# Kernel optimization log

Measured on AMD Instinct MI355X. Metric: run time of the kernel, lower is better.

Reference implementation:

```python
import jax, jax.numpy as jnp
import numpy as np

INV_SQRT2 = 0.7071067811865476


def _dense(x, W):
    return jax.nn.silu(x @ W)


def _residual(x, Wa, Wb):
    # GemNet ResidualLayer: two activated dense layers, skip, 1/sqrt(2) rescale
    return (x + _dense(_dense(x, Wa), Wb)) * INV_SQRT2


def setup_inputs() -> dict:
    key = jax.random.key(0)
    ks = iter(jax.random.split(key, 40))
    N, E, T = 10000, 200000, 400000
    NR, NS = 128, 7          # num_radial, num_spherical
    A, M, Ti, To, C = 128, 256, 64, 64, 16
    NB = 2                   # num_blocks

    def w(shape):
        fan_in = shape[-2]
        return jax.random.normal(next(ks), shape, jnp.float32) / float(np.sqrt(fan_in))

    inp = {}
    inp['atomic_numbers'] = jax.random.randint(next(ks), (N,), 0, 120)
    inp['idx_s'] = jax.random.randint(next(ks), (E,), 0, N)
    inp['idx_t'] = jax.random.randint(next(ks), (E,), 0, N)
    inp['id3_ba'] = jax.random.randint(next(ks), (T,), 0, E)
    inp['id3_ca'] = jax.random.randint(next(ks), (T,), 0, E)
    inp['rbf'] = jax.random.uniform(next(ks), (E, NR), jnp.float32)
    inp['cbf'] = jax.random.normal(next(ks), (T, NS), jnp.float32)
    V = jax.random.normal(next(ks), (E, 3), jnp.float32)
    inp['V_st'] = V / jnp.linalg.norm(V, axis=-1, keepdims=True)
    inp['atom_table'] = jax.random.normal(next(ks), (120, A), jnp.float32)
    inp['W_edge_in'] = w((2 * A + NR, M))
    inp['rbf_w3'] = w((NB, NR, M))
    inp['W_down'] = w((NB, M, Ti))
    inp['W_cbf'] = w((NB, NS, C))
    inp['W_bil'] = jax.random.normal(next(ks), (NB, C, Ti, To), jnp.float32) / float(np.sqrt(C * Ti))
    inp['W_up'] = w((NB, To, M))
    inp['W_res_e'] = w((NB, 4, M, M))
    inp['rbf_wh'] = w((NB, NR, M))
    inp['W_e2a'] = w((NB, M, A))
    inp['W_res_a'] = w((NB, 2, A, A))
    inp['W_outE_in'] = w((A * (NB + 1), A))
    inp['W_outE_res'] = w((2, A, A))
    inp['W_outE_fin'] = w((A, 1))
    inp['W_outF_in'] = w((M * (NB + 1), M))
    inp['W_outF_res'] = w((2, M, M))
    inp['W_outF_fin'] = w((M, 1))
    return inp


def reference(atomic_numbers, idx_s, idx_t, id3_ba, id3_ca, rbf, cbf, V_st,
              atom_table, W_edge_in, rbf_w3, W_down, W_cbf, W_bil, W_up,
              W_res_e, rbf_wh, W_e2a, W_res_a,
              W_outE_in, W_outE_res, W_outE_fin,
              W_outF_in, W_outF_res, W_outF_fin):
    N = atomic_numbers.shape[0]
    E = idx_s.shape[0]
    NB = rbf_w3.shape[0]

    # atom and edge embeddings
    h = atom_table[atomic_numbers]                                       # [N, A]
    m = _dense(jnp.concatenate([h[idx_s], h[idx_t], rbf], axis=-1), W_edge_in)  # [E, M]

    xs_E = [h]
    xs_F = [m]
    for b in range(NB):
        # --- triplet interaction: edge -> triplet gather, bilinear CBF mix, scatter back ---
        x = (m * (rbf @ rbf_w3[b])) @ W_down[b]                          # [E, Ti]
        cb = cbf @ W_cbf[b]                                              # [T, C]
        y = jnp.einsum('tc,ti,cio->to', cb, x[id3_ba], W_bil[b])         # [T, To]
        agg = jax.ops.segment_sum(y, id3_ca, num_segments=E)             # [E, To]
        x3 = _dense(agg @ W_up[b], jnp.eye(x3_dim := W_up[b].shape[1], dtype=m.dtype)) if False else jax.nn.silu(agg @ W_up[b])  # [E, M]
        # --- residual / skip structure ---
        m2 = _residual(m, W_res_e[b, 0], W_res_e[b, 1])
        m2 = (m2 + x3) * INV_SQRT2
        m = _residual(m2, W_res_e[b, 2], W_res_e[b, 3])
        # --- atom update: edge -> atom scatter ---
        xa = (m * (rbf @ rbf_wh[b])) @ W_e2a[b]                          # [E, A]
        ha = jax.ops.segment_sum(xa, idx_t, num_segments=N)              # [N, A]
        h = h + _residual(ha, W_res_a[b, 0], W_res_a[b, 1])
        xs_E.append(h)
        xs_F.append(m)

    # FinalMLP-style heads over concatenated per-block features (emb*(num_blocks+1))
    xE = _residual(_dense(jnp.concatenate(xs_E, axis=-1), W_outE_in), W_outE_res[0], W_outE_res[1])
    E_atom = xE @ W_outE_fin                                             # [N, 1]
    xF = _residual(_dense(jnp.concatenate(xs_F, axis=-1), W_outF_in), W_outF_res[0], W_outF_res[1])
    F_edge = xF @ W_outF_fin                                             # [E, 1]
    forces = jax.ops.segment_sum(F_edge * V_st, idx_t, num_segments=N)   # [N, 3]
    return jnp.concatenate([E_atom, forces], axis=-1)                    # [N, 4]
```

## Files before the change

### kernel.cpp

```cpp
#include <hip/hip_runtime.h>
#include <hip/hip_bf16.h>
#include <cstdio>

#define INV2 0.70710678118654752440f
typedef __hip_bfloat16 bf16;
typedef __attribute__((ext_vector_type(8))) short short8v;
typedef __attribute__((ext_vector_type(8))) unsigned short u16x8;
typedef __attribute__((ext_vector_type(4))) float f32x4;

__device__ __forceinline__ float silu_f(float v) { return v / (1.0f + __expf(-v)); }
__device__ __forceinline__ float bf2f(unsigned short u) {
    union { unsigned int i; float f; } t; t.i = ((unsigned int)u) << 16; return t.f;
}
__device__ __forceinline__ unsigned short f2bf(float x) {
    bf16 b = __float2bfloat16(x);
    return *reinterpret_cast<unsigned short*>(&b);
}
__device__ __forceinline__ float toF(float v) { return v; }
__device__ __forceinline__ float toF(bf16 v) { return __bfloat162float(v); }
__device__ __forceinline__ void stF(float* p, float v) { *p = v; }
__device__ __forceinline__ void stF(bf16* p, float v) { *p = __float2bfloat16(v); }

__device__ __forceinline__ void ld8f(const float* p, float* o) {
    const float4 a = ((const float4*)p)[0], b = ((const float4*)p)[1];
    o[0]=a.x; o[1]=a.y; o[2]=a.z; o[3]=a.w; o[4]=b.x; o[5]=b.y; o[6]=b.z; o[7]=b.w;
}
__device__ __forceinline__ void ld8f(const bf16* p, float* o) {
    const u16x8 u = *(const u16x8*)p;
#pragma unroll
    for (int j = 0; j < 8; j++) o[j] = bf2f(u[j]);
}

__device__ __forceinline__ void gll16(const void* g, void* l) {
    __builtin_amdgcn_global_load_lds(
        (const __attribute__((address_space(1))) unsigned int*)g,
        (__attribute__((address_space(3))) unsigned int*)l, 16, 0, 0);
}

enum { AM_NORMAL = 0, AM_MUL2 = 1, AM_GATHER = 2, AM_SILU = 3, AM_DMA = 4 };
enum { EP_PLAIN = 0, EP_SILU = 1, EP_ACCUM = 2, EP_RES2 = 3, EP_RESADD = 4, EP_HEADRES = 5 };

__device__ __forceinline__ float epi_val(int EPI, float v, float c, float x) {
    if (EPI == EP_PLAIN)   return v;
    if (EPI == EP_SILU)    return silu_f(v);
    if (EPI == EP_ACCUM)   return c + v;
    if (EPI == EP_RES2)    return (c + silu_f(v)) * INV2;
    if (EPI == EP_RESADD)  return c + (x + silu_f(v)) * INV2;
           return (silu_f(x) + silu_f(v)) * INV2;
}

template <int AMODE, int EPI, int BN, typename AT, typename CT>
__global__ __launch_bounds__(256) void mgemm(
    const AT* __restrict__ A, const AT* __restrict__ A2,
    const int* __restrict__ gs, const int* __restrict__ gt,
    const bf16* __restrict__ Bt,
    CT* __restrict__ C, const CT* __restrict__ X,
    int Mrows, int Ncols, int K)
{
    constexpr bool DMA = (AMODE == AM_DMA);
    constexpr int AST = DMA ? 32 : 40;
    constexpr int FM = (BN == 128) ? 4 : 2;
    __shared__ __align__(16) unsigned short Als[128 * AST];
    __shared__ __align__(16) unsigned short Bls[BN * 32];
    const int tid = threadIdx.x;
    const int row0 = blockIdx.x * 128, col0 = blockIdx.y * BN;

    const int sr = tid >> 1;
    const int sh = (tid & 1) * 16;
    const int gr = row0 + sr;
    const bool rok = (gr < Mrows);
    int is_ = 0, it_ = 0;
    if (AMODE == AM_GATHER) { if (rok) { is_ = gs[gr]; it_ = gt[gr]; } }

    const int l = tid & 63, wid = tid >> 6;
    const int lr = l & 15;
    const int lk = (l >> 4) * 8;
    const int wrow = (BN == 128) ? ((wid & 1) * 64) : (wid * 32);
    const int wcol = (BN == 128) ? ((wid >> 1) * 64) : 0;

    f32x4 acc[FM][4];
#pragma unroll
    for (int i = 0; i < FM; i++)
#pragma unroll
        for (int j = 0; j < 4; j++)
#pragma unroll
            for (int q = 0; q < 4; q++) acc[i][j][q] = 0.f;

    for (int k0 = 0; k0 < K; k0 += 32) {
        if constexpr (DMA) {
#pragma unroll
            for (int i = 0; i < 2; i++) {
                const int c = i * 256 + tid;
                const int row = c >> 2;
                if (row0 + row < Mrows)
                    gll16(A + (size_t)(row0 + row) * K + k0 + (c & 3) * 8, &Als[c * 8]);
            }
        } else {
            float va[16];
            if (rok) {
                if (AMODE == AM_GATHER) {
                    const int reg = k0 >> 7, koff = (k0 & 127) + sh;
                    const AT* src = (reg == 0) ? (A + (size_t)is_ * 128 + koff)
                                  : (reg == 1) ? (A + (size_t)it_ * 128 + koff)
                                               : (A2 + (size_t)gr * 128 + koff);
                    ld8f(src, va); ld8f(src + 8, va + 8);
                } else {
                    const AT* src = A + (size_t)gr * K + k0 + sh;
                    ld8f(src, va); ld8f(src + 8, va + 8);
                    if (AMODE == AM_MUL2) {
                        float vb[16];
                        const AT* s2 = A2 + (size_t)gr * K + k0 + sh;
                        ld8f(s2, vb); ld8f(s2 + 8, vb + 8);
#pragma unroll
                        for (int j = 0; j < 16; j++) va[j] *= vb[j];
                    } else if (AMODE == AM_SILU) {
#pragma unroll
                        for (int j = 0; j < 16; j++) va[j] = silu_f(va[j]);
                    }
                }
            } else {
#pragma unroll
                for (int j = 0; j < 16; j++) va[j] = 0.f;
            }
            u16x8 av0, av1;
#pragma unroll
            for (int j = 0; j < 8; j++) { av0[j] = f2bf(va[j]); av1[j] = f2bf(va[j + 8]); }
            *(u16x8*)&Als[sr * AST + sh] = av0;
            *(u16x8*)&Als[sr * AST + sh + 8] = av1;
        }

#pragma unroll
        for (int i = 0; i < BN / 64; i++) {
            const int c = i * 256 + tid;
            gll16(Bt + (size_t)(col0 + (c >> 2)) * K + k0 + (c & 3) * 8, &Bls[c * 8]);
        }

        __syncthreads();

        short8v af[FM], bfr[4];
#pragma unroll
        for (int fm = 0; fm < FM; fm++)
            af[fm] = *(const short8v*)&Als[(wrow + fm * 16 + lr) * AST + lk];
#pragma unroll
        for (int fn = 0; fn < 4; fn++)
            bfr[fn] = *(const short8v*)&Bls[(wcol + fn * 16 + lr) * 32 + lk];
#pragma unroll
        for (int fm = 0; fm < FM; fm++)
#pragma unroll
            for (int fn = 0; fn < 4; fn++)
                acc[fm][fn] = __builtin_amdgcn_mfma_f32_16x16x32_bf16(
                    af[fm], bfr[fn], acc[fm][fn], 0, 0, 0);

        __syncthreads();
    }

#pragma unroll
    for (int fm = 0; fm < FM; fm++) {
        const int rb = row0 + wrow + fm * 16 + (l >> 4) * 4;
#pragma unroll
        for (int fn = 0; fn < 4; fn++) {
            const int c = col0 + wcol + fn * 16 + lr;
#pragma unroll
            for (int r = 0; r < 4; r++) {
                const int rr = rb + r;
                if (rr >= Mrows) continue;
                const size_t o = (size_t)rr * Ncols + c;
                stF(&C[o], epi_val(EPI, acc[fm][fn][r],
                                   (EPI >= EP_ACCUM) ? toF(C[o]) : 0.f,
                                   (EPI == EP_RESADD || EPI == EP_HEADRES) ? toF(X[o]) : 0.f));
            }
        }
    }
}

template <int AMODE, int EPI, typename AT, typename CT>
__global__ __launch_bounds__(512) void mgemm2(
    const AT* __restrict__ A, const AT* __restrict__ A2,
    const int* __restrict__ gs, const int* __restrict__ gt,
    const bf16* __restrict__ Bt,
    CT* __restrict__ C, const CT* __restrict__ X,
    int Mrows, int K)
{
    constexpr bool DMA = (AMODE == AM_DMA);
    constexpr int AST = DMA ? 32 : 40;
    __shared__ __align__(16) unsigned short Als[2][128 * AST];
    __shared__ __align__(16) unsigned short Bls[2][256 * 32];
    const int tid = threadIdx.x;
    const int row0 = blockIdx.x * 128;

    const int sr = tid >> 2;
    const int sh = (tid & 3) * 8;
    const int gr = row0 + sr;
    const bool rok = (gr < Mrows);
    int is_ = 0, it_ = 0;
    if (AMODE == AM_GATHER) { if (rok) { is_ = gs[gr]; it_ = gt[gr]; } }

    const int l = tid & 63, wid = tid >> 6;
    const int lr = l & 15;
    const int lk = (l >> 4) * 8;
    const int wrow = (wid & 1) * 64;
    const int wcol = (wid >> 1) * 64;

    f32x4 acc[4][4];
#pragma unroll
    for (int i = 0; i < 4; i++)
#pragma unroll
        for (int j = 0; j < 4; j++)
#pragma unroll
            for (int q = 0; q < 4; q++) acc[i][j][q] = 0.f;

    auto loadA = [&](int kk, float* va) {
        if (rok) {
            if (AMODE == AM_GATHER) {
                const int reg = kk >> 7, koff = (kk & 127) + sh;
                const AT* src = (reg == 0) ? (A + (size_t)is_ * 128 + koff)
                              : (reg == 1) ? (A + (size_t)it_ * 128 + koff)
                                           : (A2 + (size_t)gr * 128 + koff);
                ld8f(src, va);
            } else {
                ld8f(A + (size_t)gr * K + kk + sh, va);
                if (AMODE == AM_MUL2) {
                    float vb[8];
                    ld8f(A2 + (size_t)gr * K + kk + sh, vb);
#pragma unroll
                    for (int j = 0; j < 8; j++) va[j] *= vb[j];
                } else if (AMODE == AM_SILU) {
#pragma unroll
                    for (int j = 0; j < 8; j++) va[j] = silu_f(va[j]);
                }
            }
        } else {
#pragma unroll
            for (int j = 0; j < 8; j++) va[j] = 0.f;
        }
    };

    for (int k0 = 0; k0 < K; k0 += 64) {
        float va0[8], va1[8];
#pragma unroll
        for (int h = 0; h < 2; h++) {
            const int kk = k0 + h * 32;
            if constexpr (DMA) {
                const int row = tid >> 2;
                if (row0 + row < Mrows)
                    gll16(A + (size_t)(row0 + row) * K + kk + (tid & 3) * 8, &Als[h][tid * 8]);
            } else {
                loadA(kk, h ? va1 : va0);
            }
#pragma unroll
            for (int i = 0; i < 2; i++) {
                const int c = i * 512 + tid;
                gll16(Bt + (size_t)(c >> 2) * K + kk + (c & 3) * 8, &Bls[h][c * 8]);
            }
        }
        if constexpr (!DMA) {
            u16x8 av0, av1;
#pragma unroll
            for (int j = 0; j < 8; j++) { av0[j] = f2bf(va0[j]); av1[j] = f2bf(va1[j]); }
            *(u16x8*)&Als[0][sr * AST + sh] = av0;
            *(u16x8*)&Als[1][sr * AST + sh] = av1;
        }

        __syncthreads();

#pragma unroll
        for (int h = 0; h < 2; h++) {
            short8v af[4], bfr[4];
#pragma unroll
            for (int fm = 0; fm < 4; fm++)
                af[fm] = *(const short8v*)&Als[h][(wrow + fm * 16 + lr) * AST + lk];
#pragma unroll
            for (int fn = 0; fn < 4; fn++)
                bfr[fn] = *(const short8v*)&Bls[h][(wcol + fn * 16 + lr) * 32 + lk];
#pragma unroll
            for (int fm = 0; fm < 4; fm++)
#pragma unroll
                for (int fn = 0; fn < 4; fn++)
                    acc[fm][fn] = __builtin_amdgcn_mfma_f32_16x16x32_bf16(
                        af[fm], bfr[fn], acc[fm][fn], 0, 0, 0);
        }

        __syncthreads();
    }

#pragma unroll
    for (int fm = 0; fm < 4; fm++) {
        const int rb = row0 + wrow + fm * 16 + (l >> 4) * 4;
#pragma unroll
        for (int fn = 0; fn < 4; fn++) {
            const int c = wcol + fn * 16 + lr;
#pragma unroll
            for (int r = 0; r < 4; r++) {
                const int rr = rb + r;
                if (rr >= Mrows) continue;
                const size_t o = (size_t)rr * 256 + c;
                stF(&C[o], epi_val(EPI, acc[fm][fn][r],
                                   (EPI >= EP_ACCUM) ? toF(C[o]) : 0.f,
                                   (EPI == EP_RESADD || EPI == EP_HEADRES) ? toF(X[o]) : 0.f));
            }
        }
    }
}

__global__ __launch_bounds__(256) void trip_gemm(
    const bf16* __restrict__ x,
    const bf16* __restrict__ cb,
    const int* __restrict__ ba, const int* __restrict__ ca,
    const bf16* __restrict__ BtT,
    float* __restrict__ agg)
{
    __shared__ __align__(16) unsigned short At[128 * 40];
    __shared__ __align__(16) unsigned short Bs[64 * 40];
    const int tid = threadIdx.x;
    const int gr0 = blockIdx.x * 128;

    const int sr = tid >> 1, sh = tid & 1;
    const int gr = gr0 + sr;
    const int e = ba[gr];
    float xr[32];
    {
        const bf16* xp = x + (size_t)e * 64 + sh * 16;
        const u16x8 a0 = *(const u16x8*)xp;
        const u16x8 a1 = *(const u16x8*)(xp + 8);
        const u16x8 b0 = *(const u16x8*)(xp + 32);
        const u16x8 b1 = *(const u16x8*)(xp + 40);
#pragma unroll
        for (int j = 0; j < 8; j++) {
            xr[j] = bf2f(a0[j]); xr[8 + j] = bf2f(a1[j]);
            xr[16 + j] = bf2f(b0[j]); xr[24 + j] = bf2f(b1[j]);
        }
    }
    float cbr[16];
    {
        const u16x8 c0 = *(const u16x8*)(cb + (size_t)gr * 16);
        const u16x8 c1 = *(const u16x8*)(cb + (size_t)gr * 16 + 8);
#pragma unroll
        for (int j = 0; j < 8; j++) { cbr[j] = bf2f(c0[j]); cbr[8 + j] = bf2f(c1[j]); }
    }

    const int l = tid & 63, wv = tid >> 6;
    const int lr = l & 15, lg = l >> 4, lk = lg * 8;
    const int wrow = wv * 32;
    const int bcol = tid >> 2, bq = tid & 3;

    f32x4 acc[2][4];
#pragma unroll
    for (int i = 0; i < 2; i++)
#pragma unroll
        for (int j = 0; j < 4; j++)
#pragma unroll
            for (int q = 0; q < 4; q++) acc[i][j][q] = 0.f;

#pragma unroll 4
    for (int ks = 0; ks < 32; ++ks) {
        const float cbv = cbr[ks >> 1];
        const int ib = (ks & 1) * 16;
        u16x8 p0, p1;
#pragma unroll
        for (int j = 0; j < 8; j++) {
            p0[j] = f2bf(cbv * xr[ib + j]);
            p1[j] = f2bf(cbv * xr[ib + 8 + j]);
        }
        *(u16x8*)&At[sr * 40 + sh * 16] = p0;
        *(u16x8*)&At[sr * 40 + sh * 16 + 8] = p1;
        const u16x8 bv8 = *(const u16x8*)(BtT + (size_t)bcol * 1024 + ks * 32 + bq * 8);
        *(u16x8*)&Bs[bcol * 40 + bq * 8] = bv8;
        __syncthreads();

        short8v af[2], bf4[4];
        af[0] = *(const short8v*)&At[(wrow + lr) * 40 + lk];
        af[1] = *(const short8v*)&At[(wrow + 16 + lr) * 40 + lk];
#pragma unroll
        for (int fn = 0; fn < 4; fn++)
            bf4[fn] = *(const short8v*)&Bs[(fn * 16 + lr) * 40 + lk];
#pragma unroll
        for (int fm = 0; fm < 2; fm++)
#pragma unroll
            for (int fn = 0; fn < 4; fn++)
                acc[fm][fn] = __builtin_amdgcn_mfma_f32_16x16x32_bf16(
                    af[fm], bf4[fn], acc[fm][fn], 0, 0, 0);
        __syncthreads();
    }

#pragma unroll
    for (int fm = 0; fm < 2; fm++)
#pragma unroll
        for (int q = 0; q < 4; q++) {
            const int rr = wrow + fm * 16 + lg * 4 + q;
            const int eo = ca[gr0 + rr];
#pragma unroll
            for (int fn = 0; fn < 4; fn++)
                atomicAdd(&agg[(size_t)eo * 64 + fn * 16 + lr], acc[fm][fn][q]);
        }
}

__global__ __launch_bounds__(256) void cb16(const float* __restrict__ cbf,
                                            const float* __restrict__ Wcb,
                                            bf16* __restrict__ cb, int T)
{
    const int gid = blockIdx.x * 256 + threadIdx.x;
    const int t = gid >> 4, c = gid & 15;
    if (t >= T) return;
    const float* cr = cbf + (size_t)t * 7;
    float s = 0.f;
#pragma unroll
    for (int k = 0; k < 7; k++) s += cr[k] * Wcb[k * 16 + c];
    cb[(size_t)t * 16 + c] = __float2bfloat16(s);
}

struct TJob { const float* src; bf16* dst; int K; int N; };
struct TJobs { TJob j[40]; };

__global__ __launch_bounds__(256) void transpose_weights(TJobs JB) {
    const TJob J = JB.j[blockIdx.y];
    const int total = J.K * J.N;
    const int gid = blockIdx.x * 256 + threadIdx.x;
    if (gid >= total) return;
    const int n = gid / J.K, k = gid - n * J.K;
    J.dst[(size_t)n * J.K + k] = __float2bfloat16(J.src[(size_t)k * J.N + n]);
}

__global__ __launch_bounds__(256) void embed_h(const int* __restrict__ z,
                                               const float* __restrict__ tab,
                                               float* __restrict__ h, int N)
{
    const int gid = blockIdx.x * 256 + threadIdx.x;
    const int n = gid >> 7, j = gid & 127;
    if (n >= N) return;
    h[(size_t)n * 128 + j] = tab[(size_t)z[n] * 128 + j];
}

__global__ __launch_bounds__(256) void scatter_ha(const bf16* __restrict__ xa,
                                                  const int* __restrict__ idxt,
                                                  float* __restrict__ ha, int E)
{
    const int gid = blockIdx.x * 256 + threadIdx.x;
    const int e = gid >> 7, j = gid & 127;
    if (e >= E) return;
    atomicAdd(&ha[(size_t)idxt[e] * 128 + j], toF(xa[(size_t)e * 128 + j]));
}

template <typename AT>
__global__ __launch_bounds__(256) void rowdot(const AT* __restrict__ Xm,
                                              const float* __restrict__ w,
                                              float* __restrict__ outv,
                                              int rows, int width, int ostride)
{
    const int wid = (blockIdx.x * 256 + threadIdx.x) >> 6;
    const int lane = threadIdx.x & 63;
    if (wid >= rows) return;
    float s = 0.f;
    for (int q = lane; q < width; q += 64) s += toF(Xm[(size_t)wid * width + q]) * w[q];
#pragma unroll
    for (int off = 32; off > 0; off >>= 1) s += __shfl_down(s, off);
    if (lane == 0) outv[(size_t)wid * ostride] = s;
}

__global__ __launch_bounds__(256) void scatter_forces(const float* __restrict__ Fe,
                                                      const float* __restrict__ Vst,
                                                      const int* __restrict__ idxt,
                                                      float* __restrict__ out, int E)
{
    const int e = blockIdx.x * 256 + threadIdx.x;
    if (e >= E) return;
    const float f = Fe[e];
    const int n = idxt[e];
    atomicAdd(&out[(size_t)n * 4 + 1], f * Vst[(size_t)e * 3 + 0]);
    atomicAdd(&out[(size_t)n * 4 + 2], f * Vst[(size_t)e * 3 + 1]);
    atomicAdd(&out[(size_t)n * 4 + 3], f * Vst[(size_t)e * 3 + 2]);
}

#define MG(AM, EP, BNv, Aptr, A2p, GS, GT, Btp, Cp, Xp, MR, NC, KK)                       \
    mgemm<AM, EP, BNv><<<dim3(((MR) + 127) / 128, (NC) / (BNv)), 256, 0, stream>>>(       \
        Aptr, A2p, GS, GT, Btp, Cp, Xp, MR, NC, KK)

#define MG2(AM, EP, Aptr, A2p, GS, GT, Btp, Cp, Xp, MR, KK)                               \
    mgemm2<AM, EP><<<((MR) + 127) / 128, 512, 0, stream>>>(                               \
        Aptr, A2p, GS, GT, Btp, Cp, Xp, MR, KK)

extern "C" void kernel_launch(void* const* d_in, const int* in_sizes, int n_in,
                              void* d_out, int out_size, void* d_ws, size_t ws_size,
                              hipStream_t stream)
{
    const int N = in_sizes[0];
    const int E = in_sizes[1];
    const int T = in_sizes[3];
    const int NB = 2;

    const int*   z        = (const int*)d_in[0];
    const int*   idx_s    = (const int*)d_in[1];
    const int*   idx_t    = (const int*)d_in[2];
    const int*   id3_ba   = (const int*)d_in[3];
    const int*   id3_ca   = (const int*)d_in[4];
    const float* rbf      = (const float*)d_in[5];
    const float* cbf      = (const float*)d_in[6];
    const float* V_st     = (const float*)d_in[7];
    const float* atom_tab = (const float*)d_in[8];
    const float* W_edge_in= (const float*)d_in[9];
    const float* rbf_w3   = (const float*)d_in[10];
    const float* W_down   = (const float*)d_in[11];
    const float* W_cbf    = (const float*)d_in[12];
    const float* W_bil    = (const float*)d_in[13];
    const float* W_up     = (const float*)d_in[14];
    const float* W_res_e  = (const float*)d_in[15];
    const float* rbf_wh   = (const float*)d_in[16];
    const float* W_e2a    = (const float*)d_in[17];
    const float* W_res_a  = (const float*)d_in[18];
    const float* W_outE_in  = (const float*)d_in[19];
    const float* W_outE_res = (const float*)d_in[20];
    const float* W_outE_fin = (const float*)d_in[21];
    const float* W_outF_in  = (const float*)d_in[22];
    const float* W_outF_res = (const float*)d_in[23];
    const float* W_outF_fin = (const float*)d_in[24];

    float* out = (float*)d_out;

    char* base = (char*)d_ws;
    size_t off = 0;
    auto alloc = [&](size_t nbytes) { char* p = base + off; off += (nbytes + 15) & ~(size_t)15; return p; };
    bf16*  m_cur = (bf16*)alloc((size_t)E * 256 * 2);
    bf16*  headF = (bf16*)alloc((size_t)E * 256 * 2);
    bf16*  S1    = (bf16*)alloc((size_t)E * 256 * 2);
    float* agg   = (float*)alloc((size_t)E * 64 * 4);
    bf16*  xbuf  = (bf16*)alloc((size_t)E * 64 * 2);
    float* h_cur = (float*)alloc((size_t)N * 128 * 4);
    float* headE = (float*)alloc((size_t)N * 128 * 4);
    float* ha    = (float*)alloc((size_t)N * 128 * 4);
    float* tA    = (float*)alloc((size_t)N * 128 * 4);
    bf16 *bt_outF[3], *bt_outE[3], *bt_r3[2], *bt_down[2], *bt_bilT[2], *bt_up[2],
         *bt_rese[8], *bt_rh[2], *bt_e2a[2], *bt_resa[4], *bt_Fres[2], *bt_Eres[2];
    bf16* bt_edge = (bf16*)alloc(384 * 256 * 2);
    for (int s = 0; s < 3; s++) bt_outF[s] = (bf16*)alloc(256 * 256 * 2);
    for (int s = 0; s < 3; s++) bt_outE[s] = (bf16*)alloc(128 * 128 * 2);
    for (int b = 0; b < 2; b++) bt_r3[b]   = (bf16*)alloc(256 * 128 * 2);
    for (int b = 0; b < 2; b++) bt_down[b] = (bf16*)alloc(64 * 256 * 2);
    for (int b = 0; b < 2; b++) bt_bilT[b] = (bf16*)alloc(64 * 1024 * 2);
    for (int b = 0; b < 2; b++) bt_up[b]   = (bf16*)alloc(256 * 64 * 2);
    for (int i = 0; i < 8; i++) bt_rese[i] = (bf16*)alloc(256 * 256 * 2);
    for (int b = 0; b < 2; b++) bt_rh[b]   = (bf16*)alloc(256 * 128 * 2);
    for (int b = 0; b < 2; b++) bt_e2a[b]  = (bf16*)alloc(128 * 256 * 2);
    for (int i = 0; i < 4; i++) bt_resa[i] = (bf16*)alloc(128 * 128 * 2);
    for (int i = 0; i < 2; i++) bt_Fres[i] = (bf16*)alloc(256 * 256 * 2);
    for (int i = 0; i < 2; i++) bt_Eres[i] = (bf16*)alloc(128 * 128 * 2);
    if (off > ws_size) {
        fprintf(stderr, "kernel_launch: ws too small: need %zu have %zu\n", off, ws_size);
        return;
    }
    bf16*  xa = (bf16*)agg;
    float* Fe = (float*)xbuf;
    float* xE = ha;
    bf16*  cbS = S1;

    const float* nfp = nullptr;
    const bf16*  nbp = nullptr;
    const int*   nip = nullptr;

    {
        TJobs JB; int nj = 0;
        auto addj = [&](const float* s, bf16* d, int K, int Nn) { JB.j[nj++] = TJob{s, d, K, Nn}; };
        addj(W_edge_in, bt_edge, 384, 256);
        for (int s = 0; s < 3; s++) addj(W_outF_in + (size_t)s * 256 * 256, bt_outF[s], 256, 256);
        for (int s = 0; s < 3; s++) addj(W_outE_in + (size_t)s * 128 * 128, bt_outE[s], 128, 128);
        for (int b = 0; b < 2; b++) addj(rbf_w3 + (size_t)b * 128 * 256, bt_r3[b], 128, 256);
        for (int b = 0; b < 2; b++) addj(W_down + (size_t)b * 256 * 64, bt_down[b], 256, 64);
        for (int b = 0; b < 2; b++) addj(W_bil + (size_t)b * 65536, bt_bilT[b], 1024, 64);
        for (int b = 0; b < 2; b++) addj(W_up + (size_t)b * 64 * 256, bt_up[b], 64, 256);
        for (int i = 0; i < 8; i++) addj(W_res_e + (size_t)i * 65536, bt_rese[i], 256, 256);
        for (int b = 0; b < 2; b++) addj(rbf_wh + (size_t)b * 128 * 256, bt_rh[b], 128, 256);
        for (int b = 0; b < 2; b++) addj(W_e2a + (size_t)b * 256 * 128, bt_e2a[b], 256, 128);
        for (int i = 0; i < 4; i++) addj(W_res_a + (size_t)i * 16384, bt_resa[i], 128, 128);
        for (int i = 0; i < 2; i++) addj(W_outF_res + (size_t)i * 65536, bt_Fres[i], 256, 256);
        for (int i = 0; i < 2; i++) addj(W_outE_res + (size_t)i * 16384, bt_Eres[i], 128, 128);
        transpose_weights<<<dim3(384, nj), 256, 0, stream>>>(JB);
    }

    embed_h<<<(N * 128 + 255) / 256, 256, 0, stream>>>(z, atom_tab, h_cur, N);
    MG2(AM_GATHER, EP_SILU, h_cur, rbf, idx_s, idx_t, bt_edge, m_cur, nbp, E, 384);
    MG2(AM_DMA, EP_PLAIN, m_cur, nbp, nip, nip, bt_outF[0], headF, nbp, E, 256);
    MG(AM_NORMAL, EP_PLAIN, 64, h_cur, nfp, nip, nip, bt_outE[0], headE, nfp, N, 128, 128);

    for (int b = 0; b < NB; ++b) {
        const float* Wcb = W_cbf + (size_t)b * 7 * 16;

        MG2(AM_NORMAL, EP_PLAIN, rbf, nfp, nip, nip, bt_r3[b], S1, nbp, E, 128);
        MG(AM_MUL2, EP_PLAIN, 64, m_cur, S1, nip, nip, bt_down[b], xbuf, nbp, E, 64, 256);
        cb16<<<(T * 16 + 255) / 256, 256, 0, stream>>>(cbf, Wcb, cbS, T);
        (void)hipMemsetAsync(agg, 0, (size_t)E * 64 * sizeof(float), stream);
        trip_gemm<<<T / 128, 256, 0, stream>>>(xbuf, cbS, id3_ba, id3_ca, bt_bilT[b], agg);

        MG2(AM_DMA, EP_SILU, m_cur, nbp, nip, nip, bt_rese[4 * b + 0], S1, nbp, E, 256);
        MG2(AM_DMA, EP_RES2, S1, nbp, nip, nip, bt_rese[4 * b + 1], m_cur, nbp, E, 256);
        MG2(AM_NORMAL, EP_RES2, agg, nfp, nip, nip, bt_up[b], m_cur, nbp, E, 64);
        MG2(AM_DMA, EP_SILU, m_cur, nbp, nip, nip, bt_rese[4 * b + 2], S1, nbp, E, 256);
        MG2(AM_DMA, EP_RES2, S1, nbp, nip, nip, bt_rese[4 * b + 3], m_cur, nbp, E, 256);
        MG2(AM_DMA, EP_ACCUM, m_cur, nbp, nip, nip, bt_outF[b + 1], headF, nbp, E, 256);

        MG2(AM_NORMAL, EP_PLAIN, rbf, nfp, nip, nip, bt_rh[b], S1, nbp, E, 128);
        MG(AM_MUL2, EP_PLAIN, 128, m_cur, S1, nip, nip, bt_e2a[b], xa, nbp, E, 128, 256);
        (void)hipMemsetAsync(ha, 0, (size_t)N * 128 * sizeof(float), stream);
        scatter_ha<<<(E * 128 + 255) / 256, 256, 0, stream>>>(xa, idx_t, ha, E);
        MG(AM_NORMAL, EP_SILU, 64, ha, nfp, nip, nip, bt_resa[2 * b + 0], tA, nfp, N, 128, 128);
        MG(AM_NORMAL, EP_RESADD, 64, tA, nfp, nip, nip, bt_resa[2 * b + 1], h_cur, ha, N, 128, 128);
        MG(AM_NORMAL, EP_ACCUM, 64, h_cur, nfp, nip, nip, bt_outE[b + 1], headE, nfp, N, 128, 128);
    }

    MG2(AM_SILU, EP_SILU, headF, nbp, nip, nip, bt_Fres[0], S1, nbp, E, 256);
    MG2(AM_DMA, EP_HEADRES, S1, nbp, nip, nip, bt_Fres[1], m_cur, headF, E, 256);
    rowdot<<<(E * 64 + 255) / 256, 256, 0, stream>>>(m_cur, W_outF_fin, Fe, E, 256, 1);

    (void)hipMemsetAsync(out, 0, (size_t)out_size * sizeof(float), stream);
    MG(AM_SILU, EP_SILU, 64, headE, nfp, nip, nip, bt_Eres[0], tA, nfp, N, 128, 128);
    MG(AM_NORMAL, EP_HEADRES, 64, tA, nfp, nip, nip, bt_Eres[1], xE, headE, N, 128, 128);
    rowdot<<<(N * 64 + 255) / 256, 256, 0, stream>>>(xE, W_outE_fin, out, N, 128, 4);
    scatter_forces<<<(E + 255) / 256, 256, 0, stream>>>(Fe, V_st, idx_t, out, E);
}
```

Baseline: 2.694 ms.

## Add register-resident A-tile GEMM for 256x256 bf16 edge layers

Adds a specialized rgemm kernel for K=256, N=256 bf16 GEMMs that loads each wave's whole A row slice into registers once and streams only B through double-buffered LDS with direct global-to-LDS loads. It replaces the generic DMA-path mgemm2 calls for the edge residual layers and head projections. The aim is to cut LDS traffic and A-staging cost. The cost is much higher register pressure, which may lower occupancy, plus a __syncthreads pair on every k-step.

Measured after the change: 3.228 ms. 1.2x slower.

```diff
diff --git a/kernel.cpp b/kernel.cpp
--- a/kernel.cpp
+++ b/kernel.cpp
@@ -302,6 +302,87 @@
     }
 }
 
+template <int EPI>
+__global__ __launch_bounds__(512) void rgemm(
+    const bf16* __restrict__ A, const bf16* __restrict__ Bt,
+    bf16* __restrict__ C, const bf16* __restrict__ X, int Mrows)
+{
+    __shared__ __align__(16) unsigned short Bls[2][256 * 32];
+    const int tid = threadIdx.x;
+    const int row0 = blockIdx.x * 128;
+    const int l = tid & 63, wv = tid >> 6;
+    const int lr = l & 15, lg = l >> 4, lk = lg * 8;
+    const int wr = (wv & 3) * 32;
+    const int wc = (wv >> 2) * 128;
+
+    u16x8 areg[2][8];
+#pragma unroll
+    for (int fm = 0; fm < 2; fm++) {
+        int row = row0 + wr + fm * 16 + lr;
+        if (row >= Mrows) row = Mrows - 1;
+        const bf16* ap = A + (size_t)row * 256 + lk;
+#pragma unroll
+        for (int ks = 0; ks < 8; ks++)
+            areg[fm][ks] = *(const u16x8*)(ap + ks * 32);
+    }
+
+    f32x4 acc[2][8];
+#pragma unroll
+    for (int i = 0; i < 2; i++)
+#pragma unroll
+        for (int j = 0; j < 8; j++)
+#pragma unroll
+            for (int q = 0; q < 4; q++) acc[i][j][q] = 0.f;
+
+    auto stageB = [&](int buf, int kk) {
+#pragma unroll
+        for (int i = 0; i < 2; i++) {
+            const int c = i * 512 + tid;
+            gll16(Bt + (size_t)(c >> 2) * 256 + kk + (c & 3) * 8, &Bls[buf][c * 8]);
+        }
+    };
+
+    for (int kp = 0; kp < 4; kp++) {
+        stageB(0, kp * 64);
+        stageB(1, kp * 64 + 32);
+        __syncthreads();
+#pragma unroll
+        for (int h = 0; h < 2; h++) {
+            short8v bfr[8];
+#pragma unroll
+            for (int fn = 0; fn < 8; fn++)
+                bfr[fn] = *(const short8v*)&Bls[h][(wc + fn * 16 + lr) * 32 + lk];
+#pragma unroll
+            for (int fm = 0; fm < 2; fm++) {
+                const short8v av = (short8v)areg[fm][kp * 2 + h];
+#pragma unroll
+                for (int fn = 0; fn < 8; fn++)
+                    acc[fm][fn] = __builtin_amdgcn_mfma_f32_16x16x32_bf16(
+                        av, bfr[fn], acc[fm][fn], 0, 0, 0);
+            }
+        }
+        __syncthreads();
+    }
+
+#pragma unroll
+    for (int fm = 0; fm < 2; fm++) {
+        const int rb = row0 + wr + fm * 16 + lg * 4;
+#pragma unroll
+        for (int fn = 0; fn < 8; fn++) {
+            const int c = wc + fn * 16 + lr;
+#pragma unroll
+            for (int q = 0; q < 4; q++) {
+                const int rr = rb + q;
+                if (rr >= Mrows) continue;
+                const size_t o = (size_t)rr * 256 + c;
+                stF(&C[o], epi_val(EPI, acc[fm][fn][q],
+                                   (EPI >= EP_ACCUM) ? toF(C[o]) : 0.f,
+                                   (EPI == EP_HEADRES) ? toF(X[o]) : 0.f));
+            }
+        }
+    }
+}
+
 __global__ __launch_bounds__(256) void trip_gemm(
     const bf16* __restrict__ x,
     const bf16* __restrict__ cb,
@@ -477,6 +558,9 @@
 #define MG2(AM, EP, Aptr, A2p, GS, GT, Btp, Cp, Xp, MR, KK)                               \
     mgemm2<AM, EP><<<((MR) + 127) / 128, 512, 0, stream>>>(                               \
         Aptr, A2p, GS, GT, Btp, Cp, Xp, MR, KK)
+
+#define RG(EP, Aptr, Btp, Cp, Xp, MR)                                                     \
+    rgemm<EP><<<((MR) + 127) / 128, 512, 0, stream>>>(Aptr, Btp, Cp, Xp, MR)
 
 extern "C" void kernel_launch(void* const* d_in, const int* in_sizes, int n_in,
                               void* d_out, int out_size, void* d_ws, size_t ws_size,
@@ -576,7 +660,7 @@
 
     embed_h<<<(N * 128 + 255) / 256, 256, 0, stream>>>(z, atom_tab, h_cur, N);
     MG2(AM_GATHER, EP_SILU, h_cur, rbf, idx_s, idx_t, bt_edge, m_cur, nbp, E, 384);
-    MG2(AM_DMA, EP_PLAIN, m_cur, nbp, nip, nip, bt_outF[0], headF, nbp, E, 256);
+    RG(EP_PLAIN, m_cur, bt_outF[0], headF, nbp, E);
     MG(AM_NORMAL, EP_PLAIN, 64, h_cur, nfp, nip, nip, bt_outE[0], headE, nfp, N, 128, 128);
 
     for (int b = 0; b < NB; ++b) {
@@ -588,12 +672,12 @@
         (void)hipMemsetAsync(agg, 0, (size_t)E * 64 * sizeof(float), stream);
         trip_gemm<<<T / 128, 256, 0, stream>>>(xbuf, cbS, id3_ba, id3_ca, bt_bilT[b], agg);
 
-        MG2(AM_DMA, EP_SILU, m_cur, nbp, nip, nip, bt_rese[4 * b + 0], S1, nbp, E, 256);
-        MG2(AM_DMA, EP_RES2, S1, nbp, nip, nip, bt_rese[4 * b + 1], m_cur, nbp, E, 256);
+        RG(EP_SILU, m_cur, bt_rese[4 * b + 0], S1, nbp, E);
+        RG(EP_RES2, S1, bt_rese[4 * b + 1], m_cur, nbp, E);
         MG2(AM_NORMAL, EP_RES2, agg, nfp, nip, nip, bt_up[b], m_cur, nbp, E, 64);
-        MG2(AM_DMA, EP_SILU, m_cur, nbp, nip, nip, bt_rese[4 * b + 2], S1, nbp, E, 256);
-        MG2(AM_DMA, EP_RES2, S1, nbp, nip, nip, bt_rese[4 * b + 3], m_cur, nbp, E, 256);
-        MG2(AM_DMA, EP_ACCUM, m_cur, nbp, nip, nip, bt_outF[b + 1], headF, nbp, E, 256);
+        RG(EP_SILU, m_cur, bt_rese[4 * b + 2], S1, nbp, E);
+        RG(EP_RES2, S1, bt_rese[4 * b + 3], m_cur, nbp, E);
+        RG(EP_ACCUM, m_cur, bt_outF[b + 1], headF, nbp, E);
 
         MG2(AM_NORMAL, EP_PLAIN, rbf, nfp, nip, nip, bt_rh[b], S1, nbp, E, 128);
         MG(AM_MUL2, EP_PLAIN, 128, m_cur, S1, nip, nip, bt_e2a[b], xa, nbp, E, 128, 256);
@@ -605,7 +689,7 @@
     }
 
     MG2(AM_SILU, EP_SILU, headF, nbp, nip, nip, bt_Fres[0], S1, nbp, E, 256);
-    MG2(AM_DMA, EP_HEADRES, S1, nbp, nip, nip, bt_Fres[1], m_cur, headF, E, 256);
+    RG(EP_HEADRES, S1, bt_Fres[1], m_cur, headF, E);
     rowdot<<<(E * 64 + 255) / 256, 256, 0, stream>>>(m_cur, W_outF_fin, Fe, E, 256, 1);
 
     (void)hipMemsetAsync(out, 0, (size_t)out_size * sizeof(float), stream);
```
